# Kernel tuning notes

Measured on AMD Instinct MI355X. Metric: run time of the kernel, lower is better.

## Reference

```python
import jax, jax.numpy as jnp
import numpy as np

D_MODEL = 1024
N_HEADS = 16
D_HEAD = D_MODEL // N_HEADS


def setup_inputs() -> dict:
    key = jax.random.key(0)
    k1, k2, k3 = jax.random.split(key, 3)
    x = jax.random.normal(k1, (4, 2048, D_MODEL), dtype=jnp.float32)
    # torch Linear(d, 3d, bias=False): y = x @ W.T with W [3d, d].
    # We store the transposed form W_qkv [d, 3d] so y = x @ W_qkv (same math).
    scale = 1.0 / np.sqrt(D_MODEL)
    W_qkv = jax.random.normal(k2, (D_MODEL, 3 * D_MODEL), dtype=jnp.float32) * scale
    W_o = jax.random.normal(k3, (D_MODEL, D_MODEL), dtype=jnp.float32) * scale
    return {"x": x, "W_qkv": W_qkv, "W_o": W_o}


def reference(x, W_qkv, W_o):
    B, T, C = x.shape
    qkv = x @ W_qkv                              # [B, T, 3C]
    Q, K, V = jnp.split(qkv, 3, axis=-1)
    def to_heads(t):
        return t.reshape(B, T, N_HEADS, D_HEAD).transpose(0, 2, 1, 3)  # [B,H,T,d]
    Q, K, V = to_heads(Q), to_heads(K), to_heads(V)
    scores = jnp.einsum("bhqd,bhkd->bhqk", Q, K) / np.sqrt(D_HEAD)
    attn = jax.nn.softmax(scores, axis=-1)
    # dropout is identity in eval/deterministic mode
    context = jnp.einsum("bhqk,bhkd->bhqd", attn, V)
    context = context.transpose(0, 2, 1, 3).reshape(B, T, C)
    return context @ W_o
```

## Files before the change

kernel.cpp:

```cpp
#include <hip/hip_runtime.h>
#include <hip/hip_bf16.h>

typedef __attribute__((ext_vector_type(8))) short short8;
typedef __attribute__((ext_vector_type(4))) short short4v;
typedef __attribute__((ext_vector_type(4))) float f32x4;
typedef __attribute__((ext_vector_type(16))) float f32x16;
typedef __attribute__((ext_vector_type(2))) unsigned int uint2v;
typedef __attribute__((ext_vector_type(4))) unsigned int uint4v;

#define SEQ    2048
#define DM     1024
#define NH     16
#define DH     64
#define NBATCH 4
#define MTOK   (NBATCH * SEQ)
#define SEG    ((size_t)NBATCH * NH * SEQ * DH)
#define QSCALE 0.18033688f

static __device__ __forceinline__ unsigned bfbits(float f) {
  unsigned u = __float_as_uint(f);
  return u + 0x7fffu + ((u >> 16) & 1u);
}
static __device__ __forceinline__ unsigned short f2bf(float f) {
  return (unsigned short)(bfbits(f) >> 16);
}
static __device__ __forceinline__ unsigned pack2bf(float lo, float hi) {
  return __builtin_amdgcn_perm(bfbits(hi), bfbits(lo), 0x07060302u);
}

typedef const __attribute__((address_space(1))) unsigned int* gp_t;
typedef __attribute__((address_space(3))) unsigned int* lp_t;
static __device__ __forceinline__ void gload_lds16(const void* g, void* l) {
  __builtin_amdgcn_global_load_lds((gp_t)g, (lp_t)l, 16, 0, 0);
}

__global__ __launch_bounds__(256) void xcast(const float* __restrict__ x,
                                             unsigned short* __restrict__ xb) {
  size_t i = ((size_t)blockIdx.x * 256 + threadIdx.x) * 8;
  f32x4 a = *(const f32x4*)&x[i];
  f32x4 b = *(const f32x4*)&x[i + 4];
  uint4v s;
  s[0] = pack2bf(a[0], a[1]);
  s[1] = pack2bf(a[2], a[3]);
  s[2] = pack2bf(b[0], b[1]);
  s[3] = pack2bf(b[2], b[3]);
  *(uint4v*)&xb[i] = s;
}

__global__ __launch_bounds__(256) void transpose_w(
    const float* __restrict__ W, unsigned short* __restrict__ WT, int K, int N) {
  __shared__ float T[64][65];
  const int tid = threadIdx.x;
  const int n0 = blockIdx.x * 64;
  const int k0 = blockIdx.y * 64;
#pragma unroll
  for (int it = 0; it < 4; it++) {
    int row = it * 16 + (tid >> 4);
    int c4 = (tid & 15) * 4;
    f32x4 v = *(const f32x4*)&W[(size_t)(k0 + row) * N + n0 + c4];
#pragma unroll
    for (int j = 0; j < 4; j++) T[row][c4 + j] = v[j];
  }
  __syncthreads();
#pragma unroll
  for (int it = 0; it < 2; it++) {
    int chunk = tid + it * 256;
    int n = chunk >> 3;
    int c8 = (chunk & 7) * 8;
    uint4v s;
#pragma unroll
    for (int j = 0; j < 4; j++)
      s[j] = pack2bf(T[c8 + 2 * j][n], T[c8 + 2 * j + 1][n]);
    *(uint4v*)&WT[(size_t)(n0 + n) * K + k0 + c8] = s;
  }
}

template <int MODE>
__global__ __launch_bounds__(256) void gemm_kernel(
    const void* __restrict__ Av, const unsigned short* __restrict__ BT,
    unsigned short* __restrict__ out0, unsigned short* __restrict__ out1,
    unsigned short* __restrict__ out2, float* __restrict__ outf,
    int M, int N, int K) {
  __shared__ unsigned short As[128][32];
  __shared__ unsigned short Bs[128][32];

  const int tid = threadIdx.x;
  const int wave = tid >> 6;
  const int lane = tid & 63;
  const int quad = lane >> 4;
  const int lc = lane & 15;
  const int wr = wave >> 1;
  const int wc = wave & 1;
  const int m0 = blockIdx.y * 128;
  const int n0 = blockIdx.x * 128;

  f32x4 acc[4][4];
#pragma unroll
  for (int i = 0; i < 4; i++)
#pragma unroll
    for (int j = 0; j < 4; j++) acc[i][j] = (f32x4){0.f, 0.f, 0.f, 0.f};

  for (int k0 = 0; k0 < K; k0 += 32) {
    if (MODE == 0) {
      const float* A = (const float*)Av;
#pragma unroll
      for (int i = 0; i < 4; i++) {
        int chunk = tid + i * 256;
        int r = chunk >> 3;
        int c4 = (chunk & 7) * 4;
        f32x4 v = *(const f32x4*)&A[(size_t)(m0 + r) * K + k0 + c4];
        uint2v s;
        s[0] = pack2bf(v[0], v[1]);
        s[1] = pack2bf(v[2], v[3]);
        *(uint2v*)&As[r][c4] = s;
      }
    } else {
      const unsigned short* A = (const unsigned short*)Av;
#pragma unroll
      for (int it = 0; it < 2; it++) {
        int rbase = wave * 32 + it * 16;
        gload_lds16(&A[(size_t)(m0 + rbase + (lane >> 2)) * K + k0 + (lane & 3) * 8],
                    &As[rbase][0]);
      }
    }
#pragma unroll
    for (int it = 0; it < 2; it++) {
      int rbase = wave * 32 + it * 16;
      gload_lds16(&BT[(size_t)(n0 + rbase + (lane >> 2)) * K + k0 + (lane & 3) * 8],
                  &Bs[rbase][0]);
    }
    __syncthreads();

    short8 aA[4], bB[4];
#pragma unroll
    for (int mt = 0; mt < 4; mt++)
      aA[mt] = *(const short8*)&As[wr * 64 + mt * 16 + lc][quad * 8];
#pragma unroll
    for (int nt = 0; nt < 4; nt++)
      bB[nt] = *(const short8*)&Bs[wc * 64 + nt * 16 + lc][quad * 8];
#pragma unroll
    for (int mt = 0; mt < 4; mt++)
#pragma unroll
      for (int nt = 0; nt < 4; nt++)
        acc[mt][nt] = __builtin_amdgcn_mfma_f32_16x16x32_bf16(
            aA[mt], bB[nt], acc[mt][nt], 0, 0, 0);
    __syncthreads();
  }

  const int c = n0 >> 10;
#pragma unroll
  for (int mt = 0; mt < 4; mt++)
#pragma unroll
    for (int nt = 0; nt < 4; nt++) {
      int rb = m0 + wr * 64 + mt * 16 + quad * 4;
      int col = n0 + wc * 64 + nt * 16 + lc;
      if (MODE == 1) {
#pragma unroll
        for (int r = 0; r < 4; r++)
          outf[(size_t)(rb + r) * N + col] = acc[mt][nt][r];
      } else {
        int rem = col & 1023;
        int h = rem >> 6;
        int dd = rem & 63;
        int b = rb >> 11;
        int tt = rb & 2047;
        if (c == 2) {
          uint2v pk;
          pk[0] = pack2bf(acc[mt][nt][0], acc[mt][nt][1]);
          pk[1] = pack2bf(acc[mt][nt][2], acc[mt][nt][3]);
          *(uint2v*)&out2[(((size_t)(b * NH + h)) * DH + dd) * SEQ + tt] = pk;
        } else {
          unsigned short* dst = (c == 0) ? out0 : out1;
          float sc = (c == 0) ? QSCALE : 1.0f;
#pragma unroll
          for (int r = 0; r < 4; r++)
            dst[(((size_t)(b * NH + h) * SEQ + tt + r) << 6) + dd] =
                f2bf(acc[mt][nt][r] * sc);
        }
      }
    }
}

__global__ __launch_bounds__(256) void attn_kernel(
    const unsigned short* __restrict__ Q, const unsigned short* __restrict__ K,
    const unsigned short* __restrict__ Vt, unsigned short* __restrict__ ctx) {
  __shared__ unsigned short KsL[64 * 64];
  __shared__ unsigned short VtL[64 * 64];
  __shared__ unsigned short Ps[4][32][72];
  __shared__ float lbuf[4][32];

  const int tid = threadIdx.x;
  const int wave = tid >> 6;
  const int lane = tid & 63;
  const int half = lane >> 5;
  const int l31 = lane & 31;
  const int bh = blockIdx.y;
  const int q0 = blockIdx.x * 128 + wave * 32;
  const size_t kqbase = (size_t)bh * SEQ * DH;
  const size_t vbase = (size_t)bh * DH * SEQ;

  short8 bQ[4];
#pragma unroll
  for (int dc = 0; dc < 4; dc++)
    bQ[dc] = *(const short8*)&Q[kqbase + (size_t)(q0 + l31) * DH + dc * 16 + half * 8];

  f32x16 o[2];
#pragma unroll
  for (int nb = 0; nb < 2; nb++)
#pragma unroll
    for (int j = 0; j < 16; j++) o[nb][j] = 0.f;
  float l_part = 0.f;

  const int xsw = l31 & 7;

  for (int kt = 0; kt < SEQ / 64; kt++) {
    const size_t kg = kqbase + (size_t)kt * 64 * DH;
    const size_t vg = vbase + (size_t)kt * 64;
#pragma unroll
    for (int it = 0; it < 2; it++) {
      int g = wave * 128 + it * 64 + lane;
      int row = g >> 3;
      int goff = ((g & 7) ^ (row & 7)) * 8;
      gload_lds16(&K[kg + (size_t)row * DH + goff],
                  &KsL[(size_t)(wave * 128 + it * 64) * 8]);
      gload_lds16(&Vt[vg + (size_t)row * SEQ + goff],
                  &VtL[(size_t)(wave * 128 + it * 64) * 8]);
    }
    __syncthreads();

#pragma unroll
    for (int kb = 0; kb < 2; kb++) {
      f32x16 s;
#pragma unroll
      for (int j = 0; j < 16; j++) s[j] = 0.f;
#pragma unroll
      for (int dc = 0; dc < 4; dc++) {
        const short8 aK = *(const short8*)&KsL[(size_t)(kb * 32 + l31) * 64 +
                                               ((dc * 2 + half) ^ xsw) * 8];
        s = __builtin_amdgcn_mfma_f32_32x32x16_bf16(aK, bQ[dc], s, 0, 0, 0);
      }
#pragma unroll
      for (int gq = 0; gq < 4; gq++) {
        float p0 = __builtin_amdgcn_exp2f(s[gq * 4 + 0]);
        float p1 = __builtin_amdgcn_exp2f(s[gq * 4 + 1]);
        float p2 = __builtin_amdgcn_exp2f(s[gq * 4 + 2]);
        float p3 = __builtin_amdgcn_exp2f(s[gq * 4 + 3]);
        l_part += (p0 + p1) + (p2 + p3);
        uint2v pk;
        pk[0] = pack2bf(p0, p1);
        pk[1] = pack2bf(p2, p3);
        *(uint2v*)&Ps[wave][l31][kb * 32 + gq * 8 + half * 4] = pk;
      }
    }

#pragma unroll
    for (int kc = 0; kc < 4; kc++) {
      const short8 pA = *(const short8*)&Ps[wave][l31][kc * 16 + half * 8];
#pragma unroll
      for (int nb = 0; nb < 2; nb++) {
        const short8 bV = *(const short8*)&VtL[(size_t)(nb * 32 + l31) * 64 +
                                               ((kc * 2 + half) ^ xsw) * 8];
        o[nb] = __builtin_amdgcn_mfma_f32_32x32x16_bf16(pA, bV, o[nb], 0, 0, 0);
      }
    }
    __syncthreads();
  }

  l_part += __shfl_xor(l_part, 32);
  lbuf[wave][l31] = 1.0f / l_part;
  __syncthreads();

  const int b = bh >> 4;
  const int h = bh & 15;
#pragma unroll
  for (int gq = 0; gq < 4; gq++)
#pragma unroll
    for (int j = 0; j < 4; j++) {
      int ql = j + gq * 8 + half * 4;
      float inv = lbuf[wave][ql];
      int token = blockIdx.x * 128 + wave * 32 + ql;
#pragma unroll
      for (int nb = 0; nb < 2; nb++)
        ctx[((size_t)b * SEQ + token) * DM + h * DH + nb * 32 + l31] =
            f2bf(o[nb][gq * 4 + j] * inv);
    }
}

extern "C" void kernel_launch(void* const* d_in, const int* in_sizes, int n_in,
                              void* d_out, int out_size, void* d_ws,
                              size_t ws_size, hipStream_t stream) {
  const float* x = (const float*)d_in[0];
  const float* Wqkv = (const float*)d_in[1];
  const float* Wo = (const float*)d_in[2];
  float* out = (float*)d_out;
  unsigned short* ws = (unsigned short*)d_ws;

  unsigned short* Qb = ws;
  unsigned short* Kb = ws + SEG;
  unsigned short* Vt = ws + 2 * SEG;
  unsigned short* Ctx = ws + 3 * SEG;
  unsigned short* WqT = Ctx + (size_t)MTOK * DM;
  unsigned short* WoT = WqT + (size_t)3 * DM * DM;
  unsigned short* Xb = WoT + (size_t)DM * DM;
  const size_t need =
      ((size_t)(Xb - ws) + (size_t)MTOK * DM) * sizeof(unsigned short);

  transpose_w<<<dim3(3 * DM / 64, DM / 64), 256, 0, stream>>>(Wqkv, WqT, DM, 3 * DM);
  transpose_w<<<dim3(DM / 64, DM / 64), 256, 0, stream>>>(Wo, WoT, DM, DM);

  if (ws_size >= need) {
    xcast<<<(MTOK * DM) / (256 * 8), 256, 0, stream>>>(x, Xb);
    gemm_kernel<2><<<dim3(3 * DM / 128, MTOK / 128), 256, 0, stream>>>(
        (const void*)Xb, WqT, Qb, Kb, Vt, nullptr, MTOK, 3 * DM, DM);
  } else {
    gemm_kernel<0><<<dim3(3 * DM / 128, MTOK / 128), 256, 0, stream>>>(
        (const void*)x, WqT, Qb, Kb, Vt, nullptr, MTOK, 3 * DM, DM);
  }
  attn_kernel<<<dim3(SEQ / 128, NBATCH * NH), 256, 0, stream>>>(Qb, Kb, Vt, Ctx);
  gemm_kernel<1><<<dim3(DM / 128, MTOK / 128), 256, 0, stream>>>(
      (const void*)Ctx, WoT, nullptr, nullptr, nullptr, out, MTOK, DM, DM);
}
```

Baseline: 297.8 us.

## Double GEMM K-step with swizzled LDS, truncate softmax probabilities, hoist attention load offsets

The GEMM kernel now stages 64-wide K slices per iteration with an XOR-swizzled LDS layout. This halves the number of barriers and is meant to avoid bank conflicts on the MFMA fragment reads. In the attention kernel, global-to-LDS load offsets are precomputed outside the loop. Probabilities are converted to bf16 by truncation instead of round-to-nearest, and the row sum uses the truncated values so it matches what goes into the P·V product. The P row stride is changed to 68 elements, so fragment reads are split into two 8-byte loads. Truncation slightly changes numerics, and the new padding can change LDS bank conflict behaviour.

```diff
diff --git a/kernel.cpp b/kernel.cpp
--- a/kernel.cpp
+++ b/kernel.cpp
@@ -2,7 +2,6 @@
 #include <hip/hip_bf16.h>
 
 typedef __attribute__((ext_vector_type(8))) short short8;
-typedef __attribute__((ext_vector_type(4))) short short4v;
 typedef __attribute__((ext_vector_type(4))) float f32x4;
 typedef __attribute__((ext_vector_type(16))) float f32x16;
 typedef __attribute__((ext_vector_type(2))) unsigned int uint2v;
@@ -26,6 +25,9 @@
 }
 static __device__ __forceinline__ unsigned pack2bf(float lo, float hi) {
   return __builtin_amdgcn_perm(bfbits(hi), bfbits(lo), 0x07060302u);
+}
+static __device__ __forceinline__ unsigned pack2tr(unsigned ulo, unsigned uhi) {
+  return __builtin_amdgcn_perm(uhi, ulo, 0x07060302u);
 }
 
 typedef const __attribute__((address_space(1))) unsigned int* gp_t;
@@ -81,8 +83,8 @@
     unsigned short* __restrict__ out0, unsigned short* __restrict__ out1,
     unsigned short* __restrict__ out2, float* __restrict__ outf,
     int M, int N, int K) {
-  __shared__ unsigned short As[128][32];
-  __shared__ unsigned short Bs[128][32];
+  __shared__ unsigned short As[128][64];
+  __shared__ unsigned short Bs[128][64];
 
   const int tid = threadIdx.x;
   const int wave = tid >> 6;
@@ -93,6 +95,9 @@
   const int wc = wave & 1;
   const int m0 = blockIdx.y * 128;
   const int n0 = blockIdx.x * 128;
+  const int xsw = lc & 7;
+  const int lr8 = lane >> 3;
+  const int sgo = ((lane & 7) ^ (lr8 & 7)) * 8;
 
   f32x4 acc[4][4];
 #pragma unroll
@@ -100,50 +105,59 @@
 #pragma unroll
     for (int j = 0; j < 4; j++) acc[i][j] = (f32x4){0.f, 0.f, 0.f, 0.f};
 
-  for (int k0 = 0; k0 < K; k0 += 32) {
+  for (int k0 = 0; k0 < K; k0 += 64) {
     if (MODE == 0) {
       const float* A = (const float*)Av;
 #pragma unroll
       for (int i = 0; i < 4; i++) {
         int chunk = tid + i * 256;
         int r = chunk >> 3;
-        int c4 = (chunk & 7) * 4;
-        f32x4 v = *(const f32x4*)&A[(size_t)(m0 + r) * K + k0 + c4];
-        uint2v s;
-        s[0] = pack2bf(v[0], v[1]);
-        s[1] = pack2bf(v[2], v[3]);
-        *(uint2v*)&As[r][c4] = s;
+        int g = chunk & 7;
+        int scol = (g ^ (r & 7)) * 8;
+        f32x4 v0 = *(const f32x4*)&A[(size_t)(m0 + r) * K + k0 + scol];
+        f32x4 v1 = *(const f32x4*)&A[(size_t)(m0 + r) * K + k0 + scol + 4];
+        uint4v s;
+        s[0] = pack2bf(v0[0], v0[1]);
+        s[1] = pack2bf(v0[2], v0[3]);
+        s[2] = pack2bf(v1[0], v1[1]);
+        s[3] = pack2bf(v1[2], v1[3]);
+        *(uint4v*)&As[r][g * 8] = s;
       }
     } else {
       const unsigned short* A = (const unsigned short*)Av;
 #pragma unroll
-      for (int it = 0; it < 2; it++) {
-        int rbase = wave * 32 + it * 16;
-        gload_lds16(&A[(size_t)(m0 + rbase + (lane >> 2)) * K + k0 + (lane & 3) * 8],
+      for (int it = 0; it < 4; it++) {
+        int rbase = wave * 32 + it * 8;
+        gload_lds16(&A[(size_t)(m0 + rbase + lr8) * K + k0 + sgo],
                     &As[rbase][0]);
       }
     }
 #pragma unroll
-    for (int it = 0; it < 2; it++) {
-      int rbase = wave * 32 + it * 16;
-      gload_lds16(&BT[(size_t)(n0 + rbase + (lane >> 2)) * K + k0 + (lane & 3) * 8],
+    for (int it = 0; it < 4; it++) {
+      int rbase = wave * 32 + it * 8;
+      gload_lds16(&BT[(size_t)(n0 + rbase + lr8) * K + k0 + sgo],
                   &Bs[rbase][0]);
     }
     __syncthreads();
 
-    short8 aA[4], bB[4];
-#pragma unroll
-    for (int mt = 0; mt < 4; mt++)
-      aA[mt] = *(const short8*)&As[wr * 64 + mt * 16 + lc][quad * 8];
-#pragma unroll
-    for (int nt = 0; nt < 4; nt++)
-      bB[nt] = *(const short8*)&Bs[wc * 64 + nt * 16 + lc][quad * 8];
-#pragma unroll
-    for (int mt = 0; mt < 4; mt++)
+#pragma unroll
+    for (int kc = 0; kc < 2; kc++) {
+      short8 aA[4], bB[4];
+#pragma unroll
+      for (int mt = 0; mt < 4; mt++)
+        aA[mt] = *(const short8*)&As[wr * 64 + mt * 16 + lc]
+                                    [((kc * 4 + quad) ^ xsw) * 8];
 #pragma unroll
       for (int nt = 0; nt < 4; nt++)
-        acc[mt][nt] = __builtin_amdgcn_mfma_f32_16x16x32_bf16(
-            aA[mt], bB[nt], acc[mt][nt], 0, 0, 0);
+        bB[nt] = *(const short8*)&Bs[wc * 64 + nt * 16 + lc]
+                                    [((kc * 4 + quad) ^ xsw) * 8];
+#pragma unroll
+      for (int mt = 0; mt < 4; mt++)
+#pragma unroll
+        for (int nt = 0; nt < 4; nt++)
+          acc[mt][nt] = __builtin_amdgcn_mfma_f32_16x16x32_bf16(
+              aA[mt], bB[nt], acc[mt][nt], 0, 0, 0);
+    }
     __syncthreads();
   }
 
@@ -186,7 +200,7 @@
     const unsigned short* __restrict__ Vt, unsigned short* __restrict__ ctx) {
   __shared__ unsigned short KsL[64 * 64];
   __shared__ unsigned short VtL[64 * 64];
-  __shared__ unsigned short Ps[4][32][72];
+  __shared__ unsigned short Ps[4][32][68];
   __shared__ float lbuf[4][32];
 
   const int tid = threadIdx.x;
@@ -212,20 +226,24 @@
   float l_part = 0.f;
 
   const int xsw = l31 & 7;
+  const int g0 = wave * 128 + lane;
+  const int r0 = g0 >> 3, r1 = (g0 + 64) >> 3;
+  const size_t so0 = (size_t)r0 * DH + (((g0 & 7) ^ (r0 & 7)) * 8);
+  const size_t so1 = (size_t)r1 * DH + (((g0 & 7) ^ (r1 & 7)) * 8);
+  const size_t sv0 = (size_t)r0 * SEQ + (((g0 & 7) ^ (r0 & 7)) * 8);
+  const size_t sv1 = (size_t)r1 * SEQ + (((g0 & 7) ^ (r1 & 7)) * 8);
+  unsigned short* ksl0 = &KsL[(size_t)(wave * 128) * 8];
+  unsigned short* ksl1 = &KsL[(size_t)(wave * 128 + 64) * 8];
+  unsigned short* vtl0 = &VtL[(size_t)(wave * 128) * 8];
+  unsigned short* vtl1 = &VtL[(size_t)(wave * 128 + 64) * 8];
 
   for (int kt = 0; kt < SEQ / 64; kt++) {
     const size_t kg = kqbase + (size_t)kt * 64 * DH;
     const size_t vg = vbase + (size_t)kt * 64;
-#pragma unroll
-    for (int it = 0; it < 2; it++) {
-      int g = wave * 128 + it * 64 + lane;
-      int row = g >> 3;
-      int goff = ((g & 7) ^ (row & 7)) * 8;
-      gload_lds16(&K[kg + (size_t)row * DH + goff],
-                  &KsL[(size_t)(wave * 128 + it * 64) * 8]);
-      gload_lds16(&Vt[vg + (size_t)row * SEQ + goff],
-                  &VtL[(size_t)(wave * 128 + it * 64) * 8]);
-    }
+    gload_lds16(&K[kg + so0], ksl0);
+    gload_lds16(&K[kg + so1], ksl1);
+    gload_lds16(&Vt[vg + sv0], vtl0);
+    gload_lds16(&Vt[vg + sv1], vtl1);
     __syncthreads();
 
 #pragma unroll
@@ -241,21 +259,29 @@
       }
 #pragma unroll
       for (int gq = 0; gq < 4; gq++) {
-        float p0 = __builtin_amdgcn_exp2f(s[gq * 4 + 0]);
-        float p1 = __builtin_amdgcn_exp2f(s[gq * 4 + 1]);
-        float p2 = __builtin_amdgcn_exp2f(s[gq * 4 + 2]);
-        float p3 = __builtin_amdgcn_exp2f(s[gq * 4 + 3]);
-        l_part += (p0 + p1) + (p2 + p3);
+        unsigned u0 = __float_as_uint(__builtin_amdgcn_exp2f(s[gq * 4 + 0]));
+        unsigned u1 = __float_as_uint(__builtin_amdgcn_exp2f(s[gq * 4 + 1]));
+        unsigned u2 = __float_as_uint(__builtin_amdgcn_exp2f(s[gq * 4 + 2]));
+        unsigned u3 = __float_as_uint(__builtin_amdgcn_exp2f(s[gq * 4 + 3]));
+        float t0 = __uint_as_float(u0 & 0xffff0000u);
+        float t1 = __uint_as_float(u1 & 0xffff0000u);
+        float t2 = __uint_as_float(u2 & 0xffff0000u);
+        float t3 = __uint_as_float(u3 & 0xffff0000u);
+        l_part += (t0 + t1) + (t2 + t3);
         uint2v pk;
-        pk[0] = pack2bf(p0, p1);
-        pk[1] = pack2bf(p2, p3);
+        pk[0] = pack2tr(u0, u1);
+        pk[1] = pack2tr(u2, u3);
         *(uint2v*)&Ps[wave][l31][kb * 32 + gq * 8 + half * 4] = pk;
       }
     }
 
 #pragma unroll
     for (int kc = 0; kc < 4; kc++) {
-      const short8 pA = *(const short8*)&Ps[wave][l31][kc * 16 + half * 8];
+      uint2v plo = *(const uint2v*)&Ps[wave][l31][kc * 16 + half * 8];
+      uint2v phi = *(const uint2v*)&Ps[wave][l31][kc * 16 + half * 8 + 4];
+      union { unsigned u[4]; short8 s8; } cv;
+      cv.u[0] = plo[0]; cv.u[1] = plo[1]; cv.u[2] = phi[0]; cv.u[3] = phi[1];
+      const short8 pA = cv.s8;
 #pragma unroll
       for (int nb = 0; nb < 2; nb++) {
         const short8 bV = *(const short8*)&VtL[(size_t)(nb * 32 + l31) * 64 +
```

New measurement: 276.9 us. 7.0% less time.
